# Performance work log

Hardware: AMD Instinct MI355X
Metric: run time of the kernel (lower is better)

The kernel has to match this reference:

```python
import jax, jax.numpy as jnp
import numpy as np

EMBED = 1024
HEADS = 16
HEAD_DIM = EMBED // HEADS


def setup_inputs() -> dict:
    key = jax.random.key(0)
    ks = jax.random.split(key, 11)
    B, S, D = 2, 2048, EMBED
    scale = 1.0 / np.sqrt(D)
    inp = {
        "q": jax.random.normal(ks[0], (B, S, D), jnp.float32),
        "k": jax.random.normal(ks[1], (B, S, D), jnp.float32),
        "v": jax.random.normal(ks[2], (B, S, D), jnp.float32),
        "Wq": jax.random.normal(ks[3], (D, D), jnp.float32) * scale,
        "bq": jnp.zeros((D,), jnp.float32),
        "Wk": jax.random.normal(ks[4], (D, D), jnp.float32) * scale,
        "bk": jnp.zeros((D,), jnp.float32),
        "Wv": jax.random.normal(ks[5], (D, D), jnp.float32) * scale,
        "bv": jnp.zeros((D,), jnp.float32),
        "Wo": jax.random.normal(ks[6], (D, D), jnp.float32) * scale,
        "bo": jnp.zeros((D,), jnp.float32),
    }
    return inp


def _split_heads(x):
    b, n, c = x.shape
    return x.reshape(b, n, HEADS, c // HEADS).transpose(0, 2, 1, 3)  # [b,h,n,dh]


def reference(q, k, v, Wq, bq, Wk, bk, Wv, bv, Wo, bo):
    qh = _split_heads(q @ Wq + bq)
    kh = _split_heads(k @ Wk + bk)
    vh = _split_heads(v @ Wv + bv)
    scale = 1.0 / jnp.sqrt(jnp.asarray(HEAD_DIM, qh.dtype))
    att = jnp.einsum("bhqd,bhkd->bhqk", qh, kh) * scale
    att = jax.nn.softmax(att, axis=-1)
    out = jnp.einsum("bhqk,bhkd->bhqd", att, vh)
    b, h, n, dh = out.shape
    out = out.transpose(0, 2, 1, 3).reshape(b, n, h * dh)
    return out @ Wo + bo
```

## Files before the change

### kernel.cpp

```cpp
#include <hip/hip_runtime.h>
#include <hip/hip_bf16.h>
#include <stdint.h>

typedef unsigned short u16;
typedef __bf16 bf16x8 __attribute__((ext_vector_type(8)));
typedef float f32x4 __attribute__((ext_vector_type(4)));
typedef unsigned int u32x4 __attribute__((ext_vector_type(4)));
typedef unsigned int u32x2 __attribute__((ext_vector_type(2)));

#define S_LEN 2048
#define DMODEL 1024
#define NHEAD 16
#define DHEAD 64
#define MROWS 4096

__device__ __forceinline__ u16 f2b(float f) {
  __hip_bfloat16 h = __float2bfloat16(f);
  union { __hip_bfloat16 h; u16 u; } c;
  c.h = h;
  return c.u;
}

__device__ __forceinline__ void gload16(const void* g, void* l) {
  __builtin_amdgcn_global_load_lds(
      (const __attribute__((address_space(1))) unsigned int*)(uintptr_t)g,
      (__attribute__((address_space(3))) unsigned int*)(uintptr_t)l,
      16, 0, 0);
}

__global__ __launch_bounds__(256) void cvt_x(const float* __restrict__ q,
                                             const float* __restrict__ k,
                                             const float* __restrict__ v,
                                             u16* __restrict__ Qx,
                                             u16* __restrict__ Kx,
                                             u16* __restrict__ Vx) {
  const int z = blockIdx.z;
  const float* src = (z == 0) ? q : (z == 1) ? k : v;
  u16* dst = (z == 0) ? Qx : (z == 1) ? Kx : Vx;
  const size_t i8 = ((size_t)blockIdx.x * 256 + threadIdx.x) * 8;
  float4 a = *(const float4*)(src + i8);
  float4 b = *(const float4*)(src + i8 + 4);
  u16 o[8];
  o[0] = f2b(a.x); o[1] = f2b(a.y); o[2] = f2b(a.z); o[3] = f2b(a.w);
  o[4] = f2b(b.x); o[5] = f2b(b.y); o[6] = f2b(b.z); o[7] = f2b(b.w);
  *(u32x4*)(dst + i8) = *(const u32x4*)o;
}

__global__ __launch_bounds__(256) void wt_t(
    const float* __restrict__ Wq, const float* __restrict__ Wk,
    const float* __restrict__ Wv, const float* __restrict__ Wo,
    u16* __restrict__ Wqt, u16* __restrict__ Wkt,
    u16* __restrict__ Wvt, u16* __restrict__ Wot) {
  const int z = blockIdx.z;
  const float* W = (z == 0) ? Wq : (z == 1) ? Wk : (z == 2) ? Wv : Wo;
  u16* Wt = (z == 0) ? Wqt : (z == 1) ? Wkt : (z == 2) ? Wvt : Wot;
  __shared__ u16 tile[64][65];
  const int n0 = blockIdx.x * 64, k0 = blockIdx.y * 64;
  const int tid = threadIdx.x;
#pragma unroll
  for (int j = 0; j < 16; j++) {
    int idx = j * 256 + tid;
    int r = idx >> 6, c = idx & 63;
    tile[r][c] = f2b(W[(size_t)(k0 + r) * DMODEL + n0 + c]);
  }
  __syncthreads();
#pragma unroll
  for (int j = 0; j < 16; j++) {
    int idx = j * 256 + tid;
    int r = idx >> 6, c = idx & 63;
    Wt[(size_t)(n0 + r) * DMODEL + k0 + c] = tile[c][r];
  }
}

__global__ __launch_bounds__(256) void v_t(const u16* __restrict__ Vp,
                                           u16* __restrict__ Vt) {
  __shared__ u16 tile[64][65];
  const int s0 = blockIdx.x * 64, h = blockIdx.y, b = blockIdx.z;
  const int tid = threadIdx.x;
#pragma unroll
  for (int j = 0; j < 16; j++) {
    int idx = j * 256 + tid;
    int r = idx >> 6, c = idx & 63;
    tile[r][c] = Vp[(size_t)(b * S_LEN + s0 + r) * DMODEL + h * DHEAD + c];
  }
  __syncthreads();
#pragma unroll
  for (int j = 0; j < 16; j++) {
    int idx = j * 256 + tid;
    int r = idx >> 6, c = idx & 63;
    Vt[(size_t)((b * NHEAD + h) * DHEAD + r) * S_LEN + s0 + c] = tile[c][r];
  }
}

template <bool F32OUT>
__device__ __forceinline__ void gemm_body(const u16* __restrict__ A,
                                          const u16* __restrict__ Bt,
                                          const float* __restrict__ bias,
                                          void* __restrict__ Cv) {
  constexpr int K = DMODEL;
  __shared__ u16 As[128 * 32];
  __shared__ u16 Bs[128 * 32];
  const int tid = threadIdx.x;
  const int wave = tid >> 6, lane = tid & 63;
  const int quad = lane >> 4, l15 = lane & 15;
  const int wr = wave >> 1, wc = wave & 1;
  const int brow = blockIdx.y, bcol = blockIdx.x;

  f32x4 acc[4][4] = {};

  for (int k0 = 0; k0 < K; k0 += 32) {
    __syncthreads();
#pragma unroll
    for (int t = 0; t < 2; t++) {
      const int slot = t * 256 + wave * 64 + lane;
      const int row = slot >> 2;
      const int col = (slot & 3) << 3;
      const int ldsb = (t * 256 + wave * 64) * 8;
      gload16(A + (size_t)(brow * 128 + row) * K + k0 + col, As + ldsb);
      gload16(Bt + (size_t)(bcol * 128 + row) * K + k0 + col, Bs + ldsb);
    }
    __syncthreads();

    bf16x8 af[4], bfm[4];
#pragma unroll
    for (int i = 0; i < 4; i++)
      af[i] = *(const bf16x8*)(As + (wr * 64 + i * 16 + l15) * 32 + quad * 8);
#pragma unroll
    for (int j = 0; j < 4; j++)
      bfm[j] = *(const bf16x8*)(Bs + (wc * 64 + j * 16 + l15) * 32 + quad * 8);
#pragma unroll
    for (int i = 0; i < 4; i++)
#pragma unroll
      for (int j = 0; j < 4; j++)
        acc[i][j] = __builtin_amdgcn_mfma_f32_16x16x32_bf16(af[i], bfm[j], acc[i][j], 0, 0, 0);
  }

#pragma unroll
  for (int i = 0; i < 4; i++)
#pragma unroll
    for (int j = 0; j < 4; j++) {
      const int col = bcol * 128 + wc * 64 + j * 16 + l15;
      const float bv = bias[col];
#pragma unroll
      for (int r = 0; r < 4; r++) {
        const int row = brow * 128 + wr * 64 + i * 16 + quad * 4 + r;
        if (F32OUT)
          ((float*)Cv)[(size_t)row * DMODEL + col] = acc[i][j][r] + bv;
        else
          ((u16*)Cv)[(size_t)row * DMODEL + col] = f2b(acc[i][j][r] + bv);
      }
    }
}

__global__ __launch_bounds__(256) void gemm_qkv(
    const u16* __restrict__ Qx, const u16* __restrict__ Kx, const u16* __restrict__ Vx,
    const u16* __restrict__ Wqt, const u16* __restrict__ Wkt, const u16* __restrict__ Wvt,
    const float* __restrict__ bq, const float* __restrict__ bk, const float* __restrict__ bv,
    u16* __restrict__ Qp, u16* __restrict__ Kp, u16* __restrict__ Vp) {
  const int z = blockIdx.z;
  const u16* A = (z == 0) ? Qx : (z == 1) ? Kx : Vx;
  const u16* Bt = (z == 0) ? Wqt : (z == 1) ? Wkt : Wvt;
  const float* bias = (z == 0) ? bq : (z == 1) ? bk : bv;
  u16* C = (z == 0) ? Qp : (z == 1) ? Kp : Vp;
  gemm_body<false>(A, Bt, bias, C);
}

__global__ __launch_bounds__(256) void gemm_out(
    const u16* __restrict__ A, const u16* __restrict__ Bt,
    const float* __restrict__ bias, float* __restrict__ C) {
  gemm_body<true>(A, Bt, bias, C);
}

#define EXP2SCALE 0.180336880112f
__global__ __launch_bounds__(256) void attn(const u16* __restrict__ Qp,
                                            const u16* __restrict__ Kp,
                                            const u16* __restrict__ Vt,
                                            u16* __restrict__ Op) {
  __shared__ u16 Ks[64 * 72];
  __shared__ u16 Vs[64 * 72];
  __shared__ u16 Ps[128 * 72];

  const int tid = threadIdx.x;
  const int wave = tid >> 6, lane = tid & 63;
  const int quad = lane >> 4, l15 = lane & 15;
  const int b = blockIdx.z, h = blockIdx.y, s0 = blockIdx.x * 128;

  const size_t baseK = ((size_t)(b * S_LEN)) * DMODEL + h * DHEAD;
  const size_t baseV = ((size_t)((b * NHEAD + h) * DHEAD)) * S_LEN;

  bf16x8 b1;
  {
    union { u16 a[8]; bf16x8 v; } c;
    u16 one = (l15 == 0) ? 0x3F80 : 0;
#pragma unroll
    for (int j = 0; j < 8; j++) c.a[j] = one;
    b1 = c.v;
  }

  bf16x8 qf[2][2];
#pragma unroll
  for (int rb = 0; rb < 2; rb++)
#pragma unroll
    for (int kx = 0; kx < 2; kx++)
      qf[rb][kx] = *(const bf16x8*)(Qp +
          ((size_t)(b * S_LEN + s0 + wave * 32 + rb * 16 + l15)) * DMODEL +
          h * DHEAD + kx * 32 + quad * 8);

  f32x4 oacc[2][4] = {};
  f32x4 lacc[2] = {};

  for (int kt = 0; kt < 32; kt++) {
    u32x4 kreg[2], vreg[2];
#pragma unroll
    for (int t = 0; t < 2; t++) {
      int idx = t * 256 + tid;
      int r = idx >> 3, c = (idx & 7) * 8;
      kreg[t] = *(const u32x4*)(Kp + baseK + (size_t)(kt * 64 + r) * DMODEL + c);
      vreg[t] = *(const u32x4*)(Vt + baseV + (size_t)r * S_LEN + kt * 64 + c);
    }
    __syncthreads();
#pragma unroll
    for (int t = 0; t < 2; t++) {
      int idx = t * 256 + tid;
      int r = idx >> 3, c = (idx & 7) * 8;
      *(u32x4*)(Ks + r * 72 + c) = kreg[t];
      *(u32x4*)(Vs + r * 72 + c) = vreg[t];
    }
    __syncthreads();

    f32x4 sfT[2][4] = {};
#pragma unroll
    for (int n = 0; n < 4; n++) {
#pragma unroll
      for (int kx = 0; kx < 2; kx++) {
        bf16x8 ka = *(const bf16x8*)(Ks + (n * 16 + l15) * 72 + kx * 32 + quad * 8);
        sfT[0][n] = __builtin_amdgcn_mfma_f32_16x16x32_bf16(ka, qf[0][kx], sfT[0][n], 0, 0, 0);
        sfT[1][n] = __builtin_amdgcn_mfma_f32_16x16x32_bf16(ka, qf[1][kx], sfT[1][n], 0, 0, 0);
      }
    }

#pragma unroll
    for (int rb = 0; rb < 2; rb++)
#pragma unroll
      for (int n = 0; n < 4; n++) {
        float p0 = __builtin_amdgcn_exp2f(sfT[rb][n][0] * EXP2SCALE);
        float p1 = __builtin_amdgcn_exp2f(sfT[rb][n][1] * EXP2SCALE);
        float p2 = __builtin_amdgcn_exp2f(sfT[rb][n][2] * EXP2SCALE);
        float p3 = __builtin_amdgcn_exp2f(sfT[rb][n][3] * EXP2SCALE);
        u32x2 pd;
        pd.x = (unsigned int)f2b(p0) | ((unsigned int)f2b(p1) << 16);
        pd.y = (unsigned int)f2b(p2) | ((unsigned int)f2b(p3) << 16);
        *(u32x2*)(Ps + (wave * 32 + rb * 16 + l15) * 72 + n * 16 + quad * 4) = pd;
      }

#pragma unroll
    for (int kx = 0; kx < 2; kx++) {
      bf16x8 ap0 = *(const bf16x8*)(Ps + (wave * 32 + l15) * 72 + kx * 32 + quad * 8);
      bf16x8 ap1 = *(const bf16x8*)(Ps + (wave * 32 + 16 + l15) * 72 + kx * 32 + quad * 8);
      lacc[0] = __builtin_amdgcn_mfma_f32_16x16x32_bf16(ap0, b1, lacc[0], 0, 0, 0);
      lacc[1] = __builtin_amdgcn_mfma_f32_16x16x32_bf16(ap1, b1, lacc[1], 0, 0, 0);
#pragma unroll
      for (int n = 0; n < 4; n++) {
        bf16x8 bv = *(const bf16x8*)(Vs + (n * 16 + l15) * 72 + kx * 32 + quad * 8);
        oacc[0][n] = __builtin_amdgcn_mfma_f32_16x16x32_bf16(ap0, bv, oacc[0][n], 0, 0, 0);
        oacc[1][n] = __builtin_amdgcn_mfma_f32_16x16x32_bf16(ap1, bv, oacc[1][n], 0, 0, 0);
      }
    }
  }

#pragma unroll
  for (int rb = 0; rb < 2; rb++) {
    float inv[4];
#pragma unroll
    for (int r = 0; r < 4; r++)
      inv[r] = 1.0f / __shfl(lacc[rb][r], quad * 16);
#pragma unroll
    for (int n = 0; n < 4; n++)
#pragma unroll
      for (int r = 0; r < 4; r++) {
        int row = s0 + wave * 32 + rb * 16 + quad * 4 + r;
        int col = h * DHEAD + n * 16 + l15;
        Op[((size_t)(b * S_LEN + row)) * DMODEL + col] = f2b(oacc[rb][n][r] * inv[r]);
      }
  }
}

extern "C" void kernel_launch(void* const* d_in, const int* in_sizes, int n_in,
                              void* d_out, int out_size, void* d_ws, size_t ws_size,
                              hipStream_t stream) {
  const float* q  = (const float*)d_in[0];
  const float* k  = (const float*)d_in[1];
  const float* v  = (const float*)d_in[2];
  const float* Wq = (const float*)d_in[3];
  const float* bq = (const float*)d_in[4];
  const float* Wk = (const float*)d_in[5];
  const float* bk = (const float*)d_in[6];
  const float* Wv = (const float*)d_in[7];
  const float* bv = (const float*)d_in[8];
  const float* Wo = (const float*)d_in[9];
  const float* bo = (const float*)d_in[10];

  char* w = (char*)d_ws;
  const size_t WSZ = (size_t)DMODEL * DMODEL * 2;
  const size_t XSZ = (size_t)MROWS * DMODEL * 2;
  u16* Wqt = (u16*)(w);
  u16* Wkt = (u16*)(w + WSZ);
  u16* Wvt = (u16*)(w + 2 * WSZ);
  u16* Wot = (u16*)(w + 3 * WSZ);
  u16* Qx  = (u16*)(w + 4 * WSZ);
  u16* Kx  = (u16*)(w + 4 * WSZ + XSZ);
  u16* Vx  = (u16*)(w + 4 * WSZ + 2 * XSZ);
  u16* Qp  = (u16*)(w + 4 * WSZ + 3 * XSZ);
  u16* Kp  = (u16*)(w + 4 * WSZ + 4 * XSZ);
  u16* Vp  = (u16*)(w + 4 * WSZ + 5 * XSZ);
  u16* Op  = (u16*)(w + 4 * WSZ + 6 * XSZ);
  u16* Vt  = Qx;

  cvt_x<<<dim3(2048, 1, 3), 256, 0, stream>>>(q, k, v, Qx, Kx, Vx);
  wt_t<<<dim3(16, 16, 4), 256, 0, stream>>>(Wq, Wk, Wv, Wo, Wqt, Wkt, Wvt, Wot);
  gemm_qkv<<<dim3(8, 32, 3), 256, 0, stream>>>(Qx, Kx, Vx, Wqt, Wkt, Wvt, bq, bk, bv, Qp, Kp, Vp);
  v_t<<<dim3(32, 16, 2), 256, 0, stream>>>(Vp, Vt);
  attn<<<dim3(16, 16, 2), 256, 0, stream>>>(Qp, Kp, Vt, Op);
  gemm_out<<<dim3(8, 32, 1), 256, 0, stream>>>(Op, Wot, bo, (float*)d_out);
}
```

Measured before the change: 241.8 us.

## Fuse prep kernels and write V projection transposed from GEMM epilogue

```diff
diff --git a/kernel.cpp b/kernel.cpp
--- a/kernel.cpp
+++ b/kernel.cpp
@@ -20,6 +20,9 @@
   c.h = h;
   return c.u;
 }
+__device__ __forceinline__ unsigned int pk2(float lo, float hi) {
+  return (unsigned int)f2b(lo) | ((unsigned int)f2b(hi) << 16);
+}
 
 __device__ __forceinline__ void gload16(const void* g, void* l) {
   __builtin_amdgcn_global_load_lds(
@@ -28,35 +31,33 @@
       16, 0, 0);
 }
 
-__global__ __launch_bounds__(256) void cvt_x(const float* __restrict__ q,
-                                             const float* __restrict__ k,
-                                             const float* __restrict__ v,
-                                             u16* __restrict__ Qx,
-                                             u16* __restrict__ Kx,
-                                             u16* __restrict__ Vx) {
-  const int z = blockIdx.z;
-  const float* src = (z == 0) ? q : (z == 1) ? k : v;
-  u16* dst = (z == 0) ? Qx : (z == 1) ? Kx : Vx;
-  const size_t i8 = ((size_t)blockIdx.x * 256 + threadIdx.x) * 8;
-  float4 a = *(const float4*)(src + i8);
-  float4 b = *(const float4*)(src + i8 + 4);
-  u16 o[8];
-  o[0] = f2b(a.x); o[1] = f2b(a.y); o[2] = f2b(a.z); o[3] = f2b(a.w);
-  o[4] = f2b(b.x); o[5] = f2b(b.y); o[6] = f2b(b.z); o[7] = f2b(b.w);
-  *(u32x4*)(dst + i8) = *(const u32x4*)o;
-}
-
-__global__ __launch_bounds__(256) void wt_t(
+__global__ __launch_bounds__(256) void prep(
+    const float* __restrict__ q, const float* __restrict__ k, const float* __restrict__ v,
     const float* __restrict__ Wq, const float* __restrict__ Wk,
     const float* __restrict__ Wv, const float* __restrict__ Wo,
+    u16* __restrict__ Qx, u16* __restrict__ Kx, u16* __restrict__ Vx,
     u16* __restrict__ Wqt, u16* __restrict__ Wkt,
     u16* __restrict__ Wvt, u16* __restrict__ Wot) {
+  __shared__ u16 tile[64][65];
   const int z = blockIdx.z;
-  const float* W = (z == 0) ? Wq : (z == 1) ? Wk : (z == 2) ? Wv : Wo;
-  u16* Wt = (z == 0) ? Wqt : (z == 1) ? Wkt : (z == 2) ? Wvt : Wot;
-  __shared__ u16 tile[64][65];
-  const int n0 = blockIdx.x * 64, k0 = blockIdx.y * 64;
   const int tid = threadIdx.x;
+  if (z < 3) {
+    const float* src = (z == 0) ? q : (z == 1) ? k : v;
+    u16* dst = (z == 0) ? Qx : (z == 1) ? Kx : Vx;
+    const size_t i8 = ((size_t)blockIdx.x * 256 + tid) * 8;
+    float4 a = *(const float4*)(src + i8);
+    float4 b = *(const float4*)(src + i8 + 4);
+    u16 o[8];
+    o[0] = f2b(a.x); o[1] = f2b(a.y); o[2] = f2b(a.z); o[3] = f2b(a.w);
+    o[4] = f2b(b.x); o[5] = f2b(b.y); o[6] = f2b(b.z); o[7] = f2b(b.w);
+    *(u32x4*)(dst + i8) = *(const u32x4*)o;
+    return;
+  }
+  if (blockIdx.x >= 256) return;
+  const int zz = z - 3;
+  const float* W = (zz == 0) ? Wq : (zz == 1) ? Wk : (zz == 2) ? Wv : Wo;
+  u16* Wt = (zz == 0) ? Wqt : (zz == 1) ? Wkt : (zz == 2) ? Wvt : Wot;
+  const int n0 = (blockIdx.x & 15) * 64, k0 = (blockIdx.x >> 4) * 64;
 #pragma unroll
   for (int j = 0; j < 16; j++) {
     int idx = j * 256 + tid;
@@ -72,27 +73,7 @@
   }
 }
 
-__global__ __launch_bounds__(256) void v_t(const u16* __restrict__ Vp,
-                                           u16* __restrict__ Vt) {
-  __shared__ u16 tile[64][65];
-  const int s0 = blockIdx.x * 64, h = blockIdx.y, b = blockIdx.z;
-  const int tid = threadIdx.x;
-#pragma unroll
-  for (int j = 0; j < 16; j++) {
-    int idx = j * 256 + tid;
-    int r = idx >> 6, c = idx & 63;
-    tile[r][c] = Vp[(size_t)(b * S_LEN + s0 + r) * DMODEL + h * DHEAD + c];
-  }
-  __syncthreads();
-#pragma unroll
-  for (int j = 0; j < 16; j++) {
-    int idx = j * 256 + tid;
-    int r = idx >> 6, c = idx & 63;
-    Vt[(size_t)((b * NHEAD + h) * DHEAD + r) * S_LEN + s0 + c] = tile[c][r];
-  }
-}
-
-template <bool F32OUT>
+template <int MODE>
 __device__ __forceinline__ void gemm_body(const u16* __restrict__ A,
                                           const u16* __restrict__ Bt,
                                           const float* __restrict__ bias,
@@ -141,13 +122,22 @@
     for (int j = 0; j < 4; j++) {
       const int col = bcol * 128 + wc * 64 + j * 16 + l15;
       const float bv = bias[col];
-#pragma unroll
-      for (int r = 0; r < 4; r++) {
-        const int row = brow * 128 + wr * 64 + i * 16 + quad * 4 + r;
-        if (F32OUT)
-          ((float*)Cv)[(size_t)row * DMODEL + col] = acc[i][j][r] + bv;
-        else
-          ((u16*)Cv)[(size_t)row * DMODEL + col] = f2b(acc[i][j][r] + bv);
+      if (MODE == 2) {
+        const int srow = brow * 128 + wr * 64 + i * 16 + quad * 4;
+        const int bb = srow >> 11, s = srow & (S_LEN - 1);
+        u32x2 pd;
+        pd.x = pk2(acc[i][j][0] + bv, acc[i][j][1] + bv);
+        pd.y = pk2(acc[i][j][2] + bv, acc[i][j][3] + bv);
+        *(u32x2*)((u16*)Cv + ((size_t)(bb * 1024 + col)) * S_LEN + s) = pd;
+      } else {
+#pragma unroll
+        for (int r = 0; r < 4; r++) {
+          const int row = brow * 128 + wr * 64 + i * 16 + quad * 4 + r;
+          if (MODE == 1)
+            ((float*)Cv)[(size_t)row * DMODEL + col] = acc[i][j][r] + bv;
+          else
+            ((u16*)Cv)[(size_t)row * DMODEL + col] = f2b(acc[i][j][r] + bv);
+        }
       }
     }
 }
@@ -156,19 +146,23 @@
     const u16* __restrict__ Qx, const u16* __restrict__ Kx, const u16* __restrict__ Vx,
     const u16* __restrict__ Wqt, const u16* __restrict__ Wkt, const u16* __restrict__ Wvt,
     const float* __restrict__ bq, const float* __restrict__ bk, const float* __restrict__ bv,
-    u16* __restrict__ Qp, u16* __restrict__ Kp, u16* __restrict__ Vp) {
+    u16* __restrict__ Qp, u16* __restrict__ Kp, u16* __restrict__ Vt) {
   const int z = blockIdx.z;
-  const u16* A = (z == 0) ? Qx : (z == 1) ? Kx : Vx;
-  const u16* Bt = (z == 0) ? Wqt : (z == 1) ? Wkt : Wvt;
-  const float* bias = (z == 0) ? bq : (z == 1) ? bk : bv;
-  u16* C = (z == 0) ? Qp : (z == 1) ? Kp : Vp;
-  gemm_body<false>(A, Bt, bias, C);
+  if (z == 2) {
+    gemm_body<2>(Vx, Wvt, bv, Vt);
+  } else {
+    const u16* A = (z == 0) ? Qx : Kx;
+    const u16* Bt = (z == 0) ? Wqt : Wkt;
+    const float* bias = (z == 0) ? bq : bk;
+    u16* C = (z == 0) ? Qp : Kp;
+    gemm_body<0>(A, Bt, bias, C);
+  }
 }
 
 __global__ __launch_bounds__(256) void gemm_out(
     const u16* __restrict__ A, const u16* __restrict__ Bt,
     const float* __restrict__ bias, float* __restrict__ C) {
-  gemm_body<true>(A, Bt, bias, C);
+  gemm_body<1>(A, Bt, bias, C);
 }
 
 #define EXP2SCALE 0.180336880112f
@@ -248,8 +242,8 @@
         float p2 = __builtin_amdgcn_exp2f(sfT[rb][n][2] * EXP2SCALE);
         float p3 = __builtin_amdgcn_exp2f(sfT[rb][n][3] * EXP2SCALE);
         u32x2 pd;
-        pd.x = (unsigned int)f2b(p0) | ((unsigned int)f2b(p1) << 16);
-        pd.y = (unsigned int)f2b(p2) | ((unsigned int)f2b(p3) << 16);
+        pd.x = pk2(p0, p1);
+        pd.y = pk2(p2, p3);
         *(u32x2*)(Ps + (wave * 32 + rb * 16 + l15) * 72 + n * 16 + quad * 4) = pd;
       }
 
@@ -312,14 +306,13 @@
   u16* Vx  = (u16*)(w + 4 * WSZ + 2 * XSZ);
   u16* Qp  = (u16*)(w + 4 * WSZ + 3 * XSZ);
   u16* Kp  = (u16*)(w + 4 * WSZ + 4 * XSZ);
-  u16* Vp  = (u16*)(w + 4 * WSZ + 5 * XSZ);
+  u16* Vt  = (u16*)(w + 4 * WSZ + 5 * XSZ);
   u16* Op  = (u16*)(w + 4 * WSZ + 6 * XSZ);
-  u16* Vt  = Qx;
-
-  cvt_x<<<dim3(2048, 1, 3), 256, 0, stream>>>(q, k, v, Qx, Kx, Vx);
-  wt_t<<<dim3(16, 16, 4), 256, 0, stream>>>(Wq, Wk, Wv, Wo, Wqt, Wkt, Wvt, Wot);
-  gemm_qkv<<<dim3(8, 32, 3), 256, 0, stream>>>(Qx, Kx, Vx, Wqt, Wkt, Wvt, bq, bk, bv, Qp, Kp, Vp);
-  v_t<<<dim3(32, 16, 2), 256, 0, stream>>>(Vp, Vt);
+
+  prep<<<dim3(2048, 1, 7), 256, 0, stream>>>(q, k, v, Wq, Wk, Wv, Wo,
+                                             Qx, Kx, Vx, Wqt, Wkt, Wvt, Wot);
+  gemm_qkv<<<dim3(8, 32, 3), 256, 0, stream>>>(Qx, Kx, Vx, Wqt, Wkt, Wvt,
+                                               bq, bk, bv, Qp, Kp, Vt);
   attn<<<dim3(16, 16, 2), 256, 0, stream>>>(Qp, Kp, Vt, Op);
   gemm_out<<<dim3(8, 32, 1), 256, 0, stream>>>(Op, Wot, bo, (float*)d_out);
 }
```

After: 236.0 us. 1.02x faster.
